# Optimization experiments

Hardware: AMD Instinct MI355X
Metric: run time of the kernel (lower is better)

## Reference

```python
import jax, jax.numpy as jnp
import numpy as np

N = 100000   # nodes
E = 1600000  # edges
EL = 200000  # decode pairs
D_IN, D_HID, D_OUT = 128, 128, 64


def setup_inputs() -> dict:
    key = jax.random.key(0)
    ks = jax.random.split(key, 9)
    x = jax.random.normal(ks[0], (N, D_IN), dtype=jnp.float32)
    edge_index = jax.random.randint(ks[1], (2, E), 0, N, dtype=jnp.int64)
    edge_label_index = jax.random.randint(ks[2], (2, EL), 0, N, dtype=jnp.int64)
    # GCNConv params: weight [in, out] (no bias inside linear), bias added after aggregation
    W1 = jax.random.normal(ks[3], (D_IN, D_HID), dtype=jnp.float32) / np.sqrt(D_IN)
    b1 = jnp.zeros((D_HID,), dtype=jnp.float32)
    W2 = jax.random.normal(ks[4], (D_HID, D_HID), dtype=jnp.float32) / np.sqrt(D_HID)
    b2 = jnp.zeros((D_HID,), dtype=jnp.float32)
    W3 = jax.random.normal(ks[5], (D_HID, D_OUT), dtype=jnp.float32) / np.sqrt(D_HID)
    b3 = jnp.zeros((D_OUT,), dtype=jnp.float32)
    return {"x": x, "edge_index": edge_index, "edge_label_index": edge_label_index,
            "W1": W1, "b1": b1, "W2": W2, "b2": b2, "W3": W3, "b3": b3}


def _gcn_norm(edge_index, num_nodes, dtype):
    # add self-loops, compute symmetric normalization deg^-1/2[src]*deg^-1/2[dst]
    loop = jnp.arange(num_nodes, dtype=edge_index.dtype)
    src = jnp.concatenate([edge_index[0], loop])
    dst = jnp.concatenate([edge_index[1], loop])
    deg = jax.ops.segment_sum(jnp.ones(src.shape, dtype=dtype), dst, num_segments=num_nodes)
    dinv = jax.lax.rsqrt(deg)  # deg >= 1 due to self-loops
    norm = dinv[src] * dinv[dst]
    return src, dst, norm


def _gcn_conv(h, W, b, src, dst, norm, num_nodes):
    h = h @ W                               # [N, out]
    msg = h[src] * norm[:, None]            # gather + scale  [E+N, out]
    out = jax.ops.segment_sum(msg, dst, num_segments=num_nodes)  # scatter-add
    return out + b


def reference(x, edge_index, edge_label_index, W1, b1, W2, b2, W3, b3):
    num_nodes = x.shape[0]
    src, dst, norm = _gcn_norm(edge_index, num_nodes, x.dtype)
    h = jax.nn.relu(_gcn_conv(x, W1, b1, src, dst, norm, num_nodes))
    h = jax.nn.relu(_gcn_conv(h, W2, b2, src, dst, norm, num_nodes))  # dropout is identity in eval
    z = _gcn_conv(h, W3, b3, src, dst, norm, num_nodes)
    # decode: dot product over candidate pairs
    return jnp.sum(z[edge_label_index[0]] * z[edge_label_index[1]], axis=-1)
```

## Files before the change

### kernel.cpp

```cpp
#include <hip/hip_runtime.h>
#include <hip/hip_bf16.h>

#define N_NODES 100000
#define N_EDGES 1600000
#define N_EL    200000

#define CPAD 16
#define GT_GEMM ((N_NODES + 63) / 64)
#define GE_RANK ((N_EDGES + 255) / 256)
#define NB2 ((N_NODES + 511) / 512)

typedef unsigned int uint32;
typedef unsigned short ushort16;
typedef __attribute__((ext_vector_type(8))) short short8;
typedef __attribute__((ext_vector_type(4))) float f32x4;

static __device__ __forceinline__ ushort16 f2bf(float f) {
    uint32 u = __float_as_uint(f);
    u += 0x7fffu + ((u >> 16) & 1u);
    return (ushort16)(u >> 16);
}
static __device__ __forceinline__ float bf_lo(uint32 p) { return __uint_as_float(p << 16); }
static __device__ __forceinline__ float bf_hi(uint32 p) { return __uint_as_float(p & 0xffff0000u); }
static __device__ __forceinline__ uint32 pack2(float lo, float hi) {
    return (uint32)f2bf(lo) | ((uint32)f2bf(hi) << 16);
}

__global__ void k_scanF(const int* __restrict__ cpad, int* __restrict__ lrp,
                        float* __restrict__ dinv, int* __restrict__ bsum,
                        int* __restrict__ boff, int* __restrict__ cnt) {
    __shared__ int s[512];
    __shared__ int lastflag;
    int t = threadIdx.x;
    int i = blockIdx.x * 512 + t;
    int v = (i < N_NODES) ? cpad[(size_t)i * CPAD] : 0;
    if (i < N_NODES) dinv[i] = rsqrtf((float)(v + 1));
    s[t] = v;
    __syncthreads();
    for (int off = 1; off < 512; off <<= 1) {
        int u = (t >= off) ? s[t - off] : 0;
        __syncthreads();
        s[t] += u;
        __syncthreads();
    }
    if (i <= N_NODES) lrp[i] = s[t] - v;
    if (t == 0) {
        __hip_atomic_store(&bsum[blockIdx.x], s[511], __ATOMIC_RELEASE,
                           __HIP_MEMORY_SCOPE_AGENT);
        int c = __hip_atomic_fetch_add(cnt, 1, __ATOMIC_ACQ_REL,
                                       __HIP_MEMORY_SCOPE_AGENT);
        lastflag = (c == NB2 - 1);
    }
    __syncthreads();
    if (!lastflag) return;
    int bv = (t < NB2) ? __hip_atomic_load(&bsum[t], __ATOMIC_ACQUIRE,
                                           __HIP_MEMORY_SCOPE_AGENT) : 0;
    s[t] = bv;
    __syncthreads();
    for (int off = 1; off < 512; off <<= 1) {
        int u = (t >= off) ? s[t - off] : 0;
        __syncthreads();
        s[t] += u;
        __syncthreads();
    }
    if (t < NB2) boff[t] = s[t] - bv;
}

__global__ void k_fill2(const int* __restrict__ src, const int* __restrict__ dst,
                        const int* __restrict__ lrp, const int* __restrict__ boff,
                        const int* __restrict__ r, int* __restrict__ col) {
    int e = blockIdx.x * blockDim.x + threadIdx.x;
    if (e >= N_EDGES) return;
    int dd = dst[e];
    int pos = lrp[dd] + boff[dd >> 9] + r[e];
    __builtin_nontemporal_store(src[e], &col[pos]);
}

static __device__ __forceinline__ short8 load_afrag(const float* arow, int off) {
    float4 a0 = *(const float4*)(arow + off);
    float4 a1 = *(const float4*)(arow + off + 4);
    short8 af;
    af[0] = (short)f2bf(a0.x); af[1] = (short)f2bf(a0.y);
    af[2] = (short)f2bf(a0.z); af[3] = (short)f2bf(a0.w);
    af[4] = (short)f2bf(a1.x); af[5] = (short)f2bf(a1.y);
    af[6] = (short)f2bf(a1.z); af[7] = (short)f2bf(a1.w);
    return af;
}
static __device__ __forceinline__ short8 load_afrag(const ushort16* arow, int off) {
    return *(const short8*)(arow + off);
}

template <int D, typename AT, bool SCALE, int OS>
static __device__ __forceinline__ void gemm_body(int bid, const AT* __restrict__ A,
        const float* __restrict__ W, const float* __restrict__ dinv,
        ushort16* __restrict__ C, short* sB) {
    constexpr int NT = D / 16;
    constexpr int LNT = (NT == 8) ? 3 : 2;
    int tid = threadIdx.x;

    constexpr int COMBOS = 4 * 4 * NT * 16;
    for (int cc = tid; cc < COMBOS; cc += 256) {
        int nn = cc & 15;
        int nt = (cc >> 4) & (NT - 1);
        int q  = (cc >> (4 + LNT)) & 3;
        int kt = cc >> (6 + LNT);
        short8 pk;
#pragma unroll
        for (int j = 0; j < 8; ++j)
            pk[j] = (short)f2bf(W[(kt * 32 + q * 8 + j) * D + nt * 16 + nn]);
        *(short8*)&sB[(((kt * NT + nt) * 64) + q * 16 + nn) * 8] = pk;
    }
    __syncthreads();

    int w = tid >> 6;
    int l = tid & 63;
    int q = l >> 4;
    int nn15 = l & 15;
    int m0 = bid * 64 + w * 16;

    f32x4 acc[NT];
#pragma unroll
    for (int i = 0; i < NT; ++i) acc[i] = (f32x4){0.f, 0.f, 0.f, 0.f};

    int m = m0 + nn15;
    m = min(m, N_NODES - 1);
    const AT* arow = A + (size_t)m * 128;

#pragma unroll
    for (int kt = 0; kt < 4; ++kt) {
        short8 af = load_afrag(arow, kt * 32 + q * 8);
#pragma unroll
        for (int nt = 0; nt < NT; ++nt) {
            short8 bf = *(const short8*)&sB[((kt * NT + nt) * 64 + l) * 8];
            acc[nt] = __builtin_amdgcn_mfma_f32_16x16x32_bf16(af, bf, acc[nt], 0, 0, 0);
        }
    }

    float4 dvv;
    if constexpr (SCALE) dvv = *(const float4*)(dinv + m0 + 4 * q);
    const float* dvp = (const float*)&dvv;
#pragma unroll
    for (int nt = 0; nt < NT; ++nt) {
#pragma unroll
        for (int rr = 0; rr < 4; ++rr) {
            int node = m0 + q * 4 + rr;
            if (node < N_NODES) {
                float val = acc[nt][rr];
                if constexpr (SCALE) val *= dvp[rr];
                C[(size_t)node * OS + nt * 16 + nn15] = f2bf(val);
            }
        }
    }
}

template <int D, typename AT, bool SCALE, int OS, bool PADZ>
__global__ __launch_bounds__(256, 5) void k_gemm_mfma(const AT* __restrict__ A,
        const float* __restrict__ W, const float* __restrict__ dinv,
        ushort16* __restrict__ C) {
    __shared__ short sB[4 * (D / 16) * 64 * 8];
    if (PADZ && blockIdx.x == 0 && threadIdx.x < OS / 2)
        ((uint32*)C)[(size_t)N_NODES * (OS / 2) + threadIdx.x] = 0;
    gemm_body<D, AT, SCALE, OS>(blockIdx.x, A, W, dinv, C, sB);
}

__global__ __launch_bounds__(256, 5) void k_fat1(const float* __restrict__ A,
        const float* __restrict__ W, ushort16* __restrict__ C,
        const int* __restrict__ dst, int* __restrict__ cpad, int* __restrict__ r) {
    __shared__ short sB[4 * 8 * 64 * 8];
    unsigned bid = blockIdx.x;
    unsigned g = bid / 5u;
    unsigned rem = bid - g * 5u;
    if (rem == 0u) {
        gemm_body<128, float, false, 128>(g, A, W, nullptr, C, sB);
    } else {
        unsigned rid = g * 4u + rem - 1u;
        unsigned e = rid * 256u + threadIdx.x;
        if (e < N_EDGES) r[e] = atomicAdd(&cpad[(size_t)dst[e] * CPAD], 1);
    }
}

template <bool RELU, bool WEIGHTED>
__global__ void k_gather128(const int* __restrict__ lrp, const int* __restrict__ boff,
                            const int* __restrict__ col, const float* __restrict__ dinv,
                            const uint32* __restrict__ t, const float* __restrict__ b,
                            uint32* __restrict__ outbuf) {
    __shared__ int   sc[4][64];
    __shared__ float sd[4][64];
    int tid = threadIdx.x;
    unsigned wid = (blockIdx.x * 256u + tid) >> 6;
    if (wid >= N_NODES) return;
    int w = tid >> 6;
    int lane = tid & 63;
    int h = lane >> 5;
    int k = lane & 31;
    int beg = lrp[wid] + boff[wid >> 9];
    int end = lrp[wid + 1] + boff[(wid + 1) >> 9];
    float di = dinv[wid];
    float a0 = 0.f, a1 = 0.f, a2 = 0.f, a3 = 0.f;
    if (h == 0) {
        uint2 p = ((const uint2*)(t + (size_t)wid * 64))[k];
        float sw = WEIGHTED ? di : 1.0f;
        a0 = sw * bf_lo(p.x); a1 = sw * bf_hi(p.x);
        a2 = sw * bf_lo(p.y); a3 = sw * bf_hi(p.y);
    }
    for (int base = beg; base < end; base += 64) {
        int cnt = min(end - base, 64);
        int c = WEIGHTED ? 0 : N_NODES;
        if (lane < cnt) c = col[base + lane];
        sc[w][lane] = c;
        if (WEIGHTED) sd[w][lane] = (lane < cnt) ? dinv[c] : 0.f;
        int nb8 = (cnt + 7) >> 3;
        for (int j8 = 0; j8 < nb8; ++j8) {
            int j = j8 << 3;
            int r0 = sc[w][j + 0 + h];
            int r1 = sc[w][j + 2 + h];
            int r2 = sc[w][j + 4 + h];
            int r3 = sc[w][j + 6 + h];
            uint2 v0 = ((const uint2*)(t + (size_t)r0 * 64))[k];
            uint2 v1 = ((const uint2*)(t + (size_t)r1 * 64))[k];
            uint2 v2 = ((const uint2*)(t + (size_t)r2 * 64))[k];
            uint2 v3 = ((const uint2*)(t + (size_t)r3 * 64))[k];
            if (WEIGHTED) {
                float d0 = sd[w][j + 0 + h];
                float d1 = sd[w][j + 2 + h];
                float d2 = sd[w][j + 4 + h];
                float d3 = sd[w][j + 6 + h];
                a0 = fmaf(d0, bf_lo(v0.x), a0); a1 = fmaf(d0, bf_hi(v0.x), a1);
                a2 = fmaf(d0, bf_lo(v0.y), a2); a3 = fmaf(d0, bf_hi(v0.y), a3);
                a0 = fmaf(d1, bf_lo(v1.x), a0); a1 = fmaf(d1, bf_hi(v1.x), a1);
                a2 = fmaf(d1, bf_lo(v1.y), a2); a3 = fmaf(d1, bf_hi(v1.y), a3);
                a0 = fmaf(d2, bf_lo(v2.x), a0); a1 = fmaf(d2, bf_hi(v2.x), a1);
                a2 = fmaf(d2, bf_lo(v2.y), a2); a3 = fmaf(d2, bf_hi(v2.y), a3);
                a0 = fmaf(d3, bf_lo(v3.x), a0); a1 = fmaf(d3, bf_hi(v3.x), a1);
                a2 = fmaf(d3, bf_lo(v3.y), a2); a3 = fmaf(d3, bf_hi(v3.y), a3);
            } else {
                a0 += (bf_lo(v0.x) + bf_lo(v1.x)) + (bf_lo(v2.x) + bf_lo(v3.x));
                a1 += (bf_hi(v0.x) + bf_hi(v1.x)) + (bf_hi(v2.x) + bf_hi(v3.x));
                a2 += (bf_lo(v0.y) + bf_lo(v1.y)) + (bf_lo(v2.y) + bf_lo(v3.y));
                a3 += (bf_hi(v0.y) + bf_hi(v1.y)) + (bf_hi(v2.y) + bf_hi(v3.y));
            }
        }
    }
    a0 += __shfl_xor(a0, 32);
    a1 += __shfl_xor(a1, 32);
    a2 += __shfl_xor(a2, 32);
    a3 += __shfl_xor(a3, 32);
    if (h == 0) {
        float4 bb = ((const float4*)b)[k];
        float o0 = fmaf(di, a0, bb.x);
        float o1 = fmaf(di, a1, bb.y);
        float o2 = fmaf(di, a2, bb.z);
        float o3 = fmaf(di, a3, bb.w);
        if (RELU) {
            o0 = fmaxf(o0, 0.f); o1 = fmaxf(o1, 0.f);
            o2 = fmaxf(o2, 0.f); o3 = fmaxf(o3, 0.f);
        }
        unsigned long long pv = (unsigned long long)pack2(o0, o1)
                              | ((unsigned long long)pack2(o2, o3) << 32);
        __builtin_nontemporal_store(pv,
            (unsigned long long*)(outbuf + (size_t)wid * 64) + k);
    }
}

__global__ void k_gather64(const int* __restrict__ lrp, const int* __restrict__ boff,
                           const int* __restrict__ col, const float* __restrict__ dinv,
                           const uint32* __restrict__ z, const float* __restrict__ b,
                           uint32* __restrict__ outbuf) {
    __shared__ int sc[4][64];
    int tid = threadIdx.x;
    unsigned wid = (blockIdx.x * 256u + tid) >> 6;
    if (wid >= N_NODES) return;
    int w = tid >> 6;
    int lane = tid & 63;
    int h = lane >> 4;
    int k = lane & 15;
    int beg = lrp[wid] + boff[wid >> 9];
    int end = lrp[wid + 1] + boff[(wid + 1) >> 9];
    float a0 = 0.f, a1 = 0.f, a2 = 0.f, a3 = 0.f;
    if (h == 0) {
        uint2 p = ((const uint2*)(z + (size_t)wid * 32))[k];
        a0 = bf_lo(p.x); a1 = bf_hi(p.x); a2 = bf_lo(p.y); a3 = bf_hi(p.y);
    }
    for (int base = beg; base < end; base += 64) {
        int cnt = min(end - base, 64);
        int c = N_NODES;
        if (lane < cnt) c = col[base + lane];
        sc[w][lane] = c;
        int nb8 = (cnt + 7) >> 3;
        for (int j8 = 0; j8 < nb8; ++j8) {
            int j = j8 << 3;
            int r0 = sc[w][j + h];
            int r1 = sc[w][j + 4 + h];
            uint2 v0 = ((const uint2*)(z + (size_t)r0 * 32))[k];
            uint2 v1 = ((const uint2*)(z + (size_t)r1 * 32))[k];
            a0 += bf_lo(v0.x) + bf_lo(v1.x);
            a1 += bf_hi(v0.x) + bf_hi(v1.x);
            a2 += bf_lo(v0.y) + bf_lo(v1.y);
            a3 += bf_hi(v0.y) + bf_hi(v1.y);
        }
    }
    a0 += __shfl_xor(a0, 16); a0 += __shfl_xor(a0, 32);
    a1 += __shfl_xor(a1, 16); a1 += __shfl_xor(a1, 32);
    a2 += __shfl_xor(a2, 16); a2 += __shfl_xor(a2, 32);
    a3 += __shfl_xor(a3, 16); a3 += __shfl_xor(a3, 32);
    if (h == 0) {
        float di = dinv[wid];
        float4 bb = ((const float4*)b)[k];
        float o0 = fmaf(di, a0, bb.x);
        float o1 = fmaf(di, a1, bb.y);
        float o2 = fmaf(di, a2, bb.z);
        float o3 = fmaf(di, a3, bb.w);
        unsigned long long pv = (unsigned long long)pack2(o0, o1)
                              | ((unsigned long long)pack2(o2, o3) << 32);
        __builtin_nontemporal_store(pv,
            (unsigned long long*)(outbuf + (size_t)wid * 32) + k);
    }
}

__global__ void k_decode(const int* __restrict__ eli, const ushort16* __restrict__ z,
                         float* __restrict__ out) {
    int e = blockIdx.x * blockDim.x + threadIdx.x;
    if (e >= N_EL) return;
    int a = eli[e];
    int b = eli[N_EL + e];
    const uint4* za = (const uint4*)(z + (size_t)a * 64);
    const uint4* zb = (const uint4*)(z + (size_t)b * 64);
    float acc = 0.0f;
#pragma unroll
    for (int i = 0; i < 8; ++i) {
        uint4 va = za[i], vb = zb[i];
        acc += bf_lo(va.x) * bf_lo(vb.x) + bf_hi(va.x) * bf_hi(vb.x);
        acc += bf_lo(va.y) * bf_lo(vb.y) + bf_hi(va.y) * bf_hi(vb.y);
        acc += bf_lo(va.z) * bf_lo(vb.z) + bf_hi(va.z) * bf_hi(vb.z);
        acc += bf_lo(va.w) * bf_lo(vb.w) + bf_hi(va.w) * bf_hi(vb.w);
    }
    out[e] = acc;
}

extern "C" void kernel_launch(void* const* d_in, const int* in_sizes, int n_in,
                              void* d_out, int out_size, void* d_ws, size_t ws_size,
                              hipStream_t stream) {
    const float* x   = (const float*)d_in[0];
    const int*   ei  = (const int*)d_in[1];
    const int*   eli = (const int*)d_in[2];
    const float* W1  = (const float*)d_in[3];
    const float* b1  = (const float*)d_in[4];
    const float* W2  = (const float*)d_in[5];
    const float* b2  = (const float*)d_in[6];
    const float* W3  = (const float*)d_in[7];
    const float* b3  = (const float*)d_in[8];
    float* out = (float*)d_out;

    const int* srcA = ei;
    const int* dstA = ei + N_EDGES;

    char* ws = (char*)d_ws;
    float*    dinv   = (float*)   (ws + 0);
    int*      lrp    = (int*)     (ws + (1024u << 10));
    int*      bsum   = (int*)     (ws + (1888u << 10));
    int*      boff   = (int*)     (ws + (1896u << 10));
    int*      col    = (int*)     (ws + (2048u << 10));
    int*      r      = (int*)     (ws + (9u << 20));
    ushort16* t      = (ushort16*)(ws + (16u << 20));
    ushort16* aggb   = (ushort16*)(ws + (48u << 20));
    int*      cpad   = (int*)     (ws + (80u << 20));
    int*      cnt    = cpad + (size_t)N_NODES * CPAD;

    const int B = 256;
    const int gG  = (N_NODES * 64 + B - 1) / B;
    const int gEL = (N_EL + B - 1) / B;

    hipMemsetAsync(cpad, 0, ((size_t)N_NODES * CPAD + 16) * sizeof(int), stream);
    hipMemsetAsync((char*)t + (size_t)N_NODES * 256, 0, 256, stream);
    k_fat1<<<GT_GEMM + GE_RANK, B, 0, stream>>>(x, W1, t, dstA, cpad, r);
    k_scanF<<<NB2, 512, 0, stream>>>(cpad, lrp, dinv, bsum, boff, cnt);
    k_fill2<<<GE_RANK, B, 0, stream>>>(srcA, dstA, lrp, boff, r, col);

    k_gather128<true, true><<<gG, B, 0, stream>>>(lrp, boff, col, dinv,
                                                  (const uint32*)t, b1, (uint32*)aggb);
    k_gemm_mfma<128, ushort16, true, 128, false><<<GT_GEMM, B, 0, stream>>>(
        aggb, W2, dinv, t);
    k_gather128<true, false><<<gG, B, 0, stream>>>(lrp, boff, col, dinv,
                                                   (const uint32*)t, b2, (uint32*)aggb);
    k_gemm_mfma<64, ushort16, true, 64, true><<<GT_GEMM, B, 0, stream>>>(
        aggb, W3, dinv, t);
    k_gather64<<<gG, B, 0, stream>>>(lrp, boff, col, dinv, (const uint32*)t, b3,
                                     (uint32*)aggb);

    k_decode<<<gEL, B, 0, stream>>>(eli, aggb, out);
}
```

Measured before the change: 444.0 us.

## Widen gather loads to 16B, unpad degree counters, fold pad-row zeroing into kernel

The degree counter array drops its 16-int padding per node. This shrinks the memset and the scan read, at the cost of more atomic contention on shared cache lines. The gather kernels now use 16-byte uint4 loads per lane with 8 accumulators instead of 8-byte loads, so more rows are in flight per wave but fewer per lane. The separate memset that zeroed the padding row of t is replaced by a store from one edge-ranking block inside k_fat1. That block is not ordered with the GEMM blocks writing t, though the pad row is separate from the rows they write.

Result: no change. 439.3 us (-1.0%).

```diff
diff --git a/kernel.cpp b/kernel.cpp
--- a/kernel.cpp
+++ b/kernel.cpp
@@ -5,7 +5,7 @@
 #define N_EDGES 1600000
 #define N_EL    200000
 
-#define CPAD 16
+#define CPAD 1
 #define GT_GEMM ((N_NODES + 63) / 64)
 #define GE_RANK ((N_EDGES + 255) / 256)
 #define NB2 ((N_NODES + 511) / 512)
@@ -14,6 +14,7 @@
 typedef unsigned short ushort16;
 typedef __attribute__((ext_vector_type(8))) short short8;
 typedef __attribute__((ext_vector_type(4))) float f32x4;
+typedef __attribute__((ext_vector_type(4))) unsigned int u32x4;
 
 static __device__ __forceinline__ ushort16 f2bf(float f) {
     uint32 u = __float_as_uint(f);
@@ -33,7 +34,7 @@
     __shared__ int lastflag;
     int t = threadIdx.x;
     int i = blockIdx.x * 512 + t;
-    int v = (i < N_NODES) ? cpad[(size_t)i * CPAD] : 0;
+    int v = (i < N_NODES) ? cpad[i] : 0;
     if (i < N_NODES) dinv[i] = rsqrtf((float)(v + 1));
     s[t] = v;
     __syncthreads();
@@ -173,9 +174,11 @@
     if (rem == 0u) {
         gemm_body<128, float, false, 128>(g, A, W, nullptr, C, sB);
     } else {
+        if (bid == 1u && threadIdx.x < 64)
+            ((uint32*)C)[(size_t)N_NODES * 64 + threadIdx.x] = 0;
         unsigned rid = g * 4u + rem - 1u;
         unsigned e = rid * 256u + threadIdx.x;
-        if (e < N_EDGES) r[e] = atomicAdd(&cpad[(size_t)dst[e] * CPAD], 1);
+        if (e < N_EDGES) r[e] = atomicAdd(&cpad[dst[e]], 1);
     }
 }
 
@@ -191,17 +194,20 @@
     if (wid >= N_NODES) return;
     int w = tid >> 6;
     int lane = tid & 63;
-    int h = lane >> 5;
-    int k = lane & 31;
+    int h = lane >> 4;
+    int k = lane & 15;
     int beg = lrp[wid] + boff[wid >> 9];
     int end = lrp[wid + 1] + boff[(wid + 1) >> 9];
     float di = dinv[wid];
     float a0 = 0.f, a1 = 0.f, a2 = 0.f, a3 = 0.f;
+    float a4 = 0.f, a5 = 0.f, a6 = 0.f, a7 = 0.f;
     if (h == 0) {
-        uint2 p = ((const uint2*)(t + (size_t)wid * 64))[k];
+        uint4 p = ((const uint4*)(t + (size_t)wid * 64))[k];
         float sw = WEIGHTED ? di : 1.0f;
         a0 = sw * bf_lo(p.x); a1 = sw * bf_hi(p.x);
         a2 = sw * bf_lo(p.y); a3 = sw * bf_hi(p.y);
+        a4 = sw * bf_lo(p.z); a5 = sw * bf_hi(p.z);
+        a6 = sw * bf_lo(p.w); a7 = sw * bf_hi(p.w);
     }
     for (int base = beg; base < end; base += 64) {
         int cnt = min(end - base, 64);
@@ -212,53 +218,62 @@
         int nb8 = (cnt + 7) >> 3;
         for (int j8 = 0; j8 < nb8; ++j8) {
             int j = j8 << 3;
-            int r0 = sc[w][j + 0 + h];
-            int r1 = sc[w][j + 2 + h];
-            int r2 = sc[w][j + 4 + h];
-            int r3 = sc[w][j + 6 + h];
-            uint2 v0 = ((const uint2*)(t + (size_t)r0 * 64))[k];
-            uint2 v1 = ((const uint2*)(t + (size_t)r1 * 64))[k];
-            uint2 v2 = ((const uint2*)(t + (size_t)r2 * 64))[k];
-            uint2 v3 = ((const uint2*)(t + (size_t)r3 * 64))[k];
+            int r0 = sc[w][j + h];
+            int r1 = sc[w][j + 4 + h];
+            uint4 v0 = ((const uint4*)(t + (size_t)r0 * 64))[k];
+            uint4 v1 = ((const uint4*)(t + (size_t)r1 * 64))[k];
             if (WEIGHTED) {
-                float d0 = sd[w][j + 0 + h];
-                float d1 = sd[w][j + 2 + h];
-                float d2 = sd[w][j + 4 + h];
-                float d3 = sd[w][j + 6 + h];
+                float d0 = sd[w][j + h];
+                float d1 = sd[w][j + 4 + h];
                 a0 = fmaf(d0, bf_lo(v0.x), a0); a1 = fmaf(d0, bf_hi(v0.x), a1);
                 a2 = fmaf(d0, bf_lo(v0.y), a2); a3 = fmaf(d0, bf_hi(v0.y), a3);
+                a4 = fmaf(d0, bf_lo(v0.z), a4); a5 = fmaf(d0, bf_hi(v0.z), a5);
+                a6 = fmaf(d0, bf_lo(v0.w), a6); a7 = fmaf(d0, bf_hi(v0.w), a7);
                 a0 = fmaf(d1, bf_lo(v1.x), a0); a1 = fmaf(d1, bf_hi(v1.x), a1);
                 a2 = fmaf(d1, bf_lo(v1.y), a2); a3 = fmaf(d1, bf_hi(v1.y), a3);
-                a0 = fmaf(d2, bf_lo(v2.x), a0); a1 = fmaf(d2, bf_hi(v2.x), a1);
-                a2 = fmaf(d2, bf_lo(v2.y), a2); a3 = fmaf(d2, bf_hi(v2.y), a3);
-                a0 = fmaf(d3, bf_lo(v3.x), a0); a1 = fmaf(d3, bf_hi(v3.x), a1);
-                a2 = fmaf(d3, bf_lo(v3.y), a2); a3 = fmaf(d3, bf_hi(v3.y), a3);
+                a4 = fmaf(d1, bf_lo(v1.z), a4); a5 = fmaf(d1, bf_hi(v1.z), a5);
+                a6 = fmaf(d1, bf_lo(v1.w), a6); a7 = fmaf(d1, bf_hi(v1.w), a7);
             } else {
-                a0 += (bf_lo(v0.x) + bf_lo(v1.x)) + (bf_lo(v2.x) + bf_lo(v3.x));
-                a1 += (bf_hi(v0.x) + bf_hi(v1.x)) + (bf_hi(v2.x) + bf_hi(v3.x));
-                a2 += (bf_lo(v0.y) + bf_lo(v1.y)) + (bf_lo(v2.y) + bf_lo(v3.y));
-                a3 += (bf_hi(v0.y) + bf_hi(v1.y)) + (bf_hi(v2.y) + bf_hi(v3.y));
+                a0 += bf_lo(v0.x) + bf_lo(v1.x);
+                a1 += bf_hi(v0.x) + bf_hi(v1.x);
+                a2 += bf_lo(v0.y) + bf_lo(v1.y);
+                a3 += bf_hi(v0.y) + bf_hi(v1.y);
+                a4 += bf_lo(v0.z) + bf_lo(v1.z);
+                a5 += bf_hi(v0.z) + bf_hi(v1.z);
+                a6 += bf_lo(v0.w) + bf_lo(v1.w);
+                a7 += bf_hi(v0.w) + bf_hi(v1.w);
             }
         }
     }
-    a0 += __shfl_xor(a0, 32);
-    a1 += __shfl_xor(a1, 32);
-    a2 += __shfl_xor(a2, 32);
-    a3 += __shfl_xor(a3, 32);
+    a0 += __shfl_xor(a0, 16); a0 += __shfl_xor(a0, 32);
+    a1 += __shfl_xor(a1, 16); a1 += __shfl_xor(a1, 32);
+    a2 += __shfl_xor(a2, 16); a2 += __shfl_xor(a2, 32);
+    a3 += __shfl_xor(a3, 16); a3 += __shfl_xor(a3, 32);
+    a4 += __shfl_xor(a4, 16); a4 += __shfl_xor(a4, 32);
+    a5 += __shfl_xor(a5, 16); a5 += __shfl_xor(a5, 32);
+    a6 += __shfl_xor(a6, 16); a6 += __shfl_xor(a6, 32);
+    a7 += __shfl_xor(a7, 16); a7 += __shfl_xor(a7, 32);
     if (h == 0) {
-        float4 bb = ((const float4*)b)[k];
-        float o0 = fmaf(di, a0, bb.x);
-        float o1 = fmaf(di, a1, bb.y);
-        float o2 = fmaf(di, a2, bb.z);
-        float o3 = fmaf(di, a3, bb.w);
+        float4 ba = ((const float4*)b)[2 * k];
+        float4 bb = ((const float4*)b)[2 * k + 1];
+        float o0 = fmaf(di, a0, ba.x);
+        float o1 = fmaf(di, a1, ba.y);
+        float o2 = fmaf(di, a2, ba.z);
+        float o3 = fmaf(di, a3, ba.w);
+        float o4 = fmaf(di, a4, bb.x);
+        float o5 = fmaf(di, a5, bb.y);
+        float o6 = fmaf(di, a6, bb.z);
+        float o7 = fmaf(di, a7, bb.w);
         if (RELU) {
             o0 = fmaxf(o0, 0.f); o1 = fmaxf(o1, 0.f);
             o2 = fmaxf(o2, 0.f); o3 = fmaxf(o3, 0.f);
+            o4 = fmaxf(o4, 0.f); o5 = fmaxf(o5, 0.f);
+            o6 = fmaxf(o6, 0.f); o7 = fmaxf(o7, 0.f);
         }
-        unsigned long long pv = (unsigned long long)pack2(o0, o1)
-                              | ((unsigned long long)pack2(o2, o3) << 32);
-        __builtin_nontemporal_store(pv,
-            (unsigned long long*)(outbuf + (size_t)wid * 64) + k);
+        u32x4 pv;
+        pv[0] = pack2(o0, o1); pv[1] = pack2(o2, o3);
+        pv[2] = pack2(o4, o5); pv[3] = pack2(o6, o7);
+        __builtin_nontemporal_store(pv, (u32x4*)(outbuf + (size_t)wid * 64) + k);
     }
 }
 
@@ -272,14 +287,16 @@
     if (wid >= N_NODES) return;
     int w = tid >> 6;
     int lane = tid & 63;
-    int h = lane >> 4;
-    int k = lane & 15;
+    int h = lane >> 3;
+    int k = lane & 7;
     int beg = lrp[wid] + boff[wid >> 9];
     int end = lrp[wid + 1] + boff[(wid + 1) >> 9];
     float a0 = 0.f, a1 = 0.f, a2 = 0.f, a3 = 0.f;
+    float a4 = 0.f, a5 = 0.f, a6 = 0.f, a7 = 0.f;
     if (h == 0) {
-        uint2 p = ((const uint2*)(z + (size_t)wid * 32))[k];
+        uint4 p = ((const uint4*)(z + (size_t)wid * 32))[k];
         a0 = bf_lo(p.x); a1 = bf_hi(p.x); a2 = bf_lo(p.y); a3 = bf_hi(p.y);
+        a4 = bf_lo(p.z); a5 = bf_hi(p.z); a6 = bf_lo(p.w); a7 = bf_hi(p.w);
     }
     for (int base = beg; base < end; base += 64) {
         int cnt = min(end - base, 64);
@@ -288,32 +305,38 @@
         sc[w][lane] = c;
         int nb8 = (cnt + 7) >> 3;
         for (int j8 = 0; j8 < nb8; ++j8) {
-            int j = j8 << 3;
-            int r0 = sc[w][j + h];
-            int r1 = sc[w][j + 4 + h];
-            uint2 v0 = ((const uint2*)(z + (size_t)r0 * 32))[k];
-            uint2 v1 = ((const uint2*)(z + (size_t)r1 * 32))[k];
-            a0 += bf_lo(v0.x) + bf_lo(v1.x);
-            a1 += bf_hi(v0.x) + bf_hi(v1.x);
-            a2 += bf_lo(v0.y) + bf_lo(v1.y);
-            a3 += bf_hi(v0.y) + bf_hi(v1.y);
+            int r0 = sc[w][(j8 << 3) + h];
+            uint4 v0 = ((const uint4*)(z + (size_t)r0 * 32))[k];
+            a0 += bf_lo(v0.x); a1 += bf_hi(v0.x);
+            a2 += bf_lo(v0.y); a3 += bf_hi(v0.y);
+            a4 += bf_lo(v0.z); a5 += bf_hi(v0.z);
+            a6 += bf_lo(v0.w); a7 += bf_hi(v0.w);
         }
     }
-    a0 += __shfl_xor(a0, 16); a0 += __shfl_xor(a0, 32);
-    a1 += __shfl_xor(a1, 16); a1 += __shfl_xor(a1, 32);
-    a2 += __shfl_xor(a2, 16); a2 += __shfl_xor(a2, 32);
-    a3 += __shfl_xor(a3, 16); a3 += __shfl_xor(a3, 32);
+    a0 += __shfl_xor(a0, 8); a0 += __shfl_xor(a0, 16); a0 += __shfl_xor(a0, 32);
+    a1 += __shfl_xor(a1, 8); a1 += __shfl_xor(a1, 16); a1 += __shfl_xor(a1, 32);
+    a2 += __shfl_xor(a2, 8); a2 += __shfl_xor(a2, 16); a2 += __shfl_xor(a2, 32);
+    a3 += __shfl_xor(a3, 8); a3 += __shfl_xor(a3, 16); a3 += __shfl_xor(a3, 32);
+    a4 += __shfl_xor(a4, 8); a4 += __shfl_xor(a4, 16); a4 += __shfl_xor(a4, 32);
+    a5 += __shfl_xor(a5, 8); a5 += __shfl_xor(a5, 16); a5 += __shfl_xor(a5, 32);
+    a6 += __shfl_xor(a6, 8); a6 += __shfl_xor(a6, 16); a6 += __shfl_xor(a6, 32);
+    a7 += __shfl_xor(a7, 8); a7 += __shfl_xor(a7, 16); a7 += __shfl_xor(a7, 32);
     if (h == 0) {
         float di = dinv[wid];
-        float4 bb = ((const float4*)b)[k];
-        float o0 = fmaf(di, a0, bb.x);
-        float o1 = fmaf(di, a1, bb.y);
-        float o2 = fmaf(di, a2, bb.z);
-        float o3 = fmaf(di, a3, bb.w);
-        unsigned long long pv = (unsigned long long)pack2(o0, o1)
-                              | ((unsigned long long)pack2(o2, o3) << 32);
-        __builtin_nontemporal_store(pv,
-            (unsigned long long*)(outbuf + (size_t)wid * 32) + k);
+        float4 ba = ((const float4*)b)[2 * k];
+        float4 bb = ((const float4*)b)[2 * k + 1];
+        float o0 = fmaf(di, a0, ba.x);
+        float o1 = fmaf(di, a1, ba.y);
+        float o2 = fmaf(di, a2, ba.z);
+        float o3 = fmaf(di, a3, ba.w);
+        float o4 = fmaf(di, a4, bb.x);
+        float o5 = fmaf(di, a5, bb.y);
+        float o6 = fmaf(di, a6, bb.z);
+        float o7 = fmaf(di, a7, bb.w);
+        u32x4 pv;
+        pv[0] = pack2(o0, o1); pv[1] = pack2(o2, o3);
+        pv[2] = pack2(o4, o5); pv[3] = pack2(o6, o7);
+        __builtin_nontemporal_store(pv, (u32x4*)(outbuf + (size_t)wid * 32) + k);
     }
 }
 
@@ -364,14 +387,13 @@
     ushort16* t      = (ushort16*)(ws + (16u << 20));
     ushort16* aggb   = (ushort16*)(ws + (48u << 20));
     int*      cpad   = (int*)     (ws + (80u << 20));
-    int*      cnt    = cpad + (size_t)N_NODES * CPAD;
+    int*      cnt    = cpad + N_NODES;
 
     const int B = 256;
     const int gG  = (N_NODES * 64 + B - 1) / B;
     const int gEL = (N_EL + B - 1) / B;
 
-    hipMemsetAsync(cpad, 0, ((size_t)N_NODES * CPAD + 16) * sizeof(int), stream);
-    hipMemsetAsync((char*)t + (size_t)N_NODES * 256, 0, 256, stream);
+    hipMemsetAsync(cpad, 0, ((size_t)N_NODES + 16) * sizeof(int), stream);
     k_fat1<<<GT_GEMM + GE_RANK, B, 0, stream>>>(x, W1, t, dstA, cpad, r);
     k_scanF<<<NB2, 512, 0, stream>>>(cpad, lrp, dinv, bsum, boff, cnt);
     k_fill2<<<GE_RANK, B, 0, stream>>>(srcA, dstA, lrp, boff, r, col);
```
